# Performance work log

Hardware: AMD Instinct MI355X
Metric: run time of the kernel (lower is better)

Reference implementation:

```python
import jax, jax.numpy as jnp
import numpy as np
from jax import lax

GO_ID = 2
EOS_ID = 3
MAX_LEN = 64
BATCH = 32
VOCAB = 32000
EMBED = 256
HIDDEN = 512


def setup_inputs() -> dict:
    key = jax.random.key(0)
    ks = jax.random.split(key, 8)
    s = 0.05  # keep logits / gates in a sane range
    return {
        "emb_table": jax.random.normal(ks[0], (VOCAB, EMBED), jnp.float32) * s,
        "W_ih": jax.random.normal(ks[1], (3 * HIDDEN, EMBED), jnp.float32) * s,
        "b_ih": jax.random.normal(ks[2], (3 * HIDDEN,), jnp.float32) * s,
        "W_hh": jax.random.normal(ks[3], (3 * HIDDEN, HIDDEN), jnp.float32) * s,
        "b_hh": jax.random.normal(ks[4], (3 * HIDDEN,), jnp.float32) * s,
        "W_out": jax.random.normal(ks[5], (VOCAB, HIDDEN), jnp.float32) * s,
        "b_out": jax.random.normal(ks[6], (VOCAB,), jnp.float32) * s,
        "h0": jax.random.normal(ks[7], (BATCH, HIDDEN), jnp.float32),
    }


def reference(emb_table, W_ih, b_ih, W_hh, b_hh, W_out, b_out, h0):
    start_id = GO_ID  # no_unk=True -> start_id = dm.go_id

    def gru_cell(x, h):
        # torch.nn.GRUCell semantics
        gi = x @ W_ih.T + b_ih            # [B, 3H]
        gh = h @ W_hh.T + b_hh            # [B, 3H]
        i_r, i_z, i_n = jnp.split(gi, 3, axis=-1)
        h_r, h_z, h_n = jnp.split(gh, 3, axis=-1)
        r = jax.nn.sigmoid(i_r + h_r)
        z = jax.nn.sigmoid(i_z + h_z)
        n = jnp.tanh(i_n + r * h_n)
        return (1.0 - z) * n + z * h

    first_emb = jnp.broadcast_to(emb_table[GO_ID], (BATCH, EMBED))
    flag0 = jnp.zeros((BATCH,), dtype=bool)

    def step(carry, _):
        h, next_emb, flag = carry
        h = gru_cell(next_emb, h)
        w = h @ W_out.T + b_out                      # logits [B, V]
        w_pro = jax.nn.softmax(w, axis=-1)
        tok = jnp.argmax(w[:, start_id:], axis=1) + start_id  # greedy, skip specials
        ne = emb_table[tok]
        eosmet = flag                                 # flag BEFORE updating (as in torch loop)
        flag = flag | (tok == EOS_ID)
        return (h, ne, flag), (w_pro, tok, ne, eosmet)

    _, (w_pro, w_o, emb_seq, EOSmet) = lax.scan(
        step, (h0, first_emb, flag0), None, length=MAX_LEN
    )
    alive = jnp.logical_not(EOSmet)                   # EOSmet = 1 - stacked flags
    w_o = w_o * alive.astype(w_o.dtype)               # zero out tokens after EOS
    emb_seq = emb_seq * alive.astype(emb_seq.dtype)[..., None]
    length = jnp.sum(alive.astype(jnp.int32), axis=0)
    return w_pro, w_o, emb_seq, length
```

## Files before the change

### kernel.cpp

```cpp
#include <hip/hip_runtime.h>
#include <math.h>

#define BB 32
#define EE 256
#define HH 512
#define VV 32000
#define TT 64
#define GO_ID 2
#define EOS_ID 3

#define NBL 500
#define NT  256

#define WS_HT0   0
#define WS_HT1   16384
#define WS_X     32768
#define WS_PART  40960
#define WS_M     104960
#define WS_SINV  104992
#define WS_INT   105024

#define OUT_WO   65536000ULL
#define OUT_EMB  (OUT_WO + 2048ULL)
#define OUT_LEN  (OUT_EMB + 524288ULL)

__global__ __launch_bounds__(NT)
void k_init(const float* __restrict__ emb, float* __restrict__ ws)
{
    float* xbuf = ws + WS_X;
    int* toki  = (int*)(ws + WS_INT);
    int* flags = toki;
    int* lenac = toki + 32;
    xbuf[blockIdx.x*EE + threadIdx.x] = emb[GO_ID*EE + threadIdx.x];
    if (blockIdx.x == 0 && threadIdx.x < BB) { flags[threadIdx.x] = 0; lenac[threadIdx.x] = 0; }
}

__global__ __launch_bounds__(NT)
void k_gru(const float* __restrict__ Wih, const float* __restrict__ bih,
           const float* __restrict__ Whh, const float* __restrict__ bhh,
           const float* __restrict__ h0, float* __restrict__ ws, int t)
{
    const int blk = blockIdx.x, tid = threadIdx.x;
    float* hTprev = ws + (((t & 1) == 0) ? WS_HT1 : WS_HT0);
    float* hTcur  = ws + (((t & 1) == 0) ? WS_HT0 : WS_HT1);
    const float* xbuf = ws + WS_X;

    __shared__ float smem[1536];

    const int b    = tid & 31;
    const int q    = tid >> 5;
    const int k    = blk*4 + (q & 3);
    const int half = q >> 2;

    float s_ir = 0.f, s_iz = 0.f, s_in = 0.f;
    {
        const float4* x4 = (const float4*)xbuf + b*64;
        const float4* wr = (const float4*)Wih + (size_t)k*64;
        const float4* wz = (const float4*)Wih + (size_t)(HH + k)*64;
        const float4* wn = (const float4*)Wih + (size_t)(2*HH + k)*64;
        const int c0 = half*32, c1 = c0 + 32;
        for (int c4 = c0; c4 < c1; ++c4) {
            float4 xv = x4[c4];
            float4 a  = wr[c4];
            s_ir += a.x*xv.x + a.y*xv.y + a.z*xv.z + a.w*xv.w;
            float4 bz = wz[c4];
            s_iz += bz.x*xv.x + bz.y*xv.y + bz.z*xv.z + bz.w*xv.w;
            float4 cn = wn[c4];
            s_in += cn.x*xv.x + cn.y*xv.y + cn.z*xv.z + cn.w*xv.w;
        }
    }
    float s_hr = 0.f, s_hz = 0.f, s_hn = 0.f;
    {
        const float4* wr = (const float4*)Whh + (size_t)k*128;
        const float4* wz = (const float4*)Whh + (size_t)(HH + k)*128;
        const float4* wn = (const float4*)Whh + (size_t)(2*HH + k)*128;
        const int c0 = half*64, c1 = c0 + 64;
        if (t == 0) {
            const float4* h4 = (const float4*)h0 + b*128;
            for (int c4 = c0; c4 < c1; ++c4) {
                float4 hv = h4[c4];
                float4 a  = wr[c4];
                s_hr += a.x*hv.x + a.y*hv.y + a.z*hv.z + a.w*hv.w;
                float4 bz = wz[c4];
                s_hz += bz.x*hv.x + bz.y*hv.y + bz.z*hv.z + bz.w*hv.w;
                float4 cn = wn[c4];
                s_hn += cn.x*hv.x + cn.y*hv.y + cn.z*hv.z + cn.w*hv.w;
            }
        } else {
            const float4* h4 = (const float4*)hTprev;
            for (int c4 = c0; c4 < c1; ++c4) {
                float4 hv = h4[c4*32 + b];
                float4 a  = wr[c4];
                s_hr += a.x*hv.x + a.y*hv.y + a.z*hv.z + a.w*hv.w;
                float4 bz = wz[c4];
                s_hz += bz.x*hv.x + bz.y*hv.y + bz.z*hv.z + bz.w*hv.w;
                float4 cn = wn[c4];
                s_hn += cn.x*hv.x + cn.y*hv.y + cn.z*hv.z + cn.w*hv.w;
            }
        }
    }
    const int si = (q*32 + b)*6;
    smem[si+0] = s_ir; smem[si+1] = s_iz; smem[si+2] = s_in;
    smem[si+3] = s_hr; smem[si+4] = s_hz; smem[si+5] = s_hn;
    __syncthreads();
    if (q < 4) {
        const int i0 = (q*32 + b)*6, i1 = ((q+4)*32 + b)*6;
        float ir  = smem[i0+0] + smem[i1+0] + bih[k];
        float iz  = smem[i0+1] + smem[i1+1] + bih[HH + k];
        float inn = smem[i0+2] + smem[i1+2] + bih[2*HH + k];
        float hr  = smem[i0+3] + smem[i1+3] + bhh[k];
        float hz  = smem[i0+4] + smem[i1+4] + bhh[HH + k];
        float hn  = smem[i0+5] + smem[i1+5] + bhh[2*HH + k];
        float r = 1.f/(1.f + expf(-(ir + hr)));
        float z = 1.f/(1.f + expf(-(iz + hz)));
        float n = tanhf(inn + r*hn);
        float hp = (t == 0) ? h0[b*HH + k] : hTprev[(k>>2)*128 + b*4 + (k&3)];
        float hv = (1.f - z)*n + z*hp;
        hTcur[(k>>2)*128 + b*4 + (k&3)] = hv;
    }
}

__global__ __launch_bounds__(NT)
void k_logits(const float* __restrict__ Wout, const float* __restrict__ bout,
              float* __restrict__ out, float* __restrict__ ws, int t)
{
    const int blk = blockIdx.x, tid = threadIdx.x;
    const float* hTcur = ws + (((t & 1) == 0) ? WS_HT0 : WS_HT1);
    float* part  = ws + WS_PART;
    const float* Mrow  = ws + WS_M;
    const float* SinvA = ws + WS_SINV;
    float* w_pro = out;

    __shared__ float smem[2080];

    if (t > 0) {
        float* wp = w_pro + (size_t)(t-1)*1024000 + blk*64;
        const int vl = tid & 63, bq = tid >> 6;
        #pragma unroll
        for (int r = 0; r < 8; ++r) {
            int b = r*4 + bq;
            size_t idx = (size_t)b*VV + vl;
            wp[idx] = expf(wp[idx] - Mrow[b]) * SinvA[b];
        }
    }

    const int b  = tid & 31;
    const int vg = tid >> 5;
    const int v0 = blk*64 + vg*8;
    float acc[8] = {0.f,0.f,0.f,0.f,0.f,0.f,0.f,0.f};
    const float4* hT4  = (const float4*)hTcur;
    const float4* wrow = (const float4*)Wout + (size_t)v0*128;
    for (int c4 = 0; c4 < 128; ++c4) {
        float4 hv = hT4[c4*32 + b];
        #pragma unroll
        for (int i = 0; i < 8; ++i) {
            float4 wv = wrow[(size_t)i*128 + c4];
            acc[i] += wv.x*hv.x + wv.y*hv.y + wv.z*hv.z + wv.w*hv.w;
        }
    }
    __syncthreads();
    #pragma unroll
    for (int i = 0; i < 8; ++i)
        smem[b*65 + vg*8 + i] = acc[i] + bout[v0 + i];
    __syncthreads();
    {
        float* wp = w_pro + (size_t)t*1024000 + blk*64;
        const int vl = tid & 63, bq = tid >> 6;
        #pragma unroll
        for (int r = 0; r < 8; ++r) {
            int b2 = r*4 + bq;
            wp[(size_t)b2*VV + vl] = smem[b2*65 + vl];
        }
    }
    {
        const int rb = tid >> 3, l = tid & 7;
        float m = -INFINITY, s = 0.f, av = -INFINITY; int ai = 0;
        for (int j = l; j < 64; j += 8) {
            float val = smem[rb*65 + j];
            if (val > m) { s = s*expf(m - val) + 1.f; m = val; }
            else         { s += expf(val - m); }
            int vglob = blk*64 + j;
            if (vglob >= 2 && val > av) { av = val; ai = vglob; }
        }
        for (int d = 1; d < 8; d <<= 1) {
            float m2  = __shfl_xor(m, d);
            float s2  = __shfl_xor(s, d);
            float av2 = __shfl_xor(av, d);
            int   ai2 = __shfl_xor(ai, d);
            float mn = fmaxf(m, m2);
            s = s*expf(m - mn) + s2*expf(m2 - mn); m = mn;
            if (av2 > av || (av2 == av && ai2 < ai)) { av = av2; ai = ai2; }
        }
        if (l == 0)
            ((float4*)part)[blk*32 + rb] = make_float4(m, s, av, __int_as_float(ai));
    }
}

__global__ __launch_bounds__(NT)
void k_reduce(const float* __restrict__ emb, float* __restrict__ out,
              float* __restrict__ ws, int t)
{
    const int b = blockIdx.x, tid = threadIdx.x;
    const float* part = ws + WS_PART;
    float* Mrow  = ws + WS_M;
    float* SinvA = ws + WS_SINV;
    int*   flags = (int*)(ws + WS_INT);
    int*   lenac = flags + 32;
    float* xbuf  = ws + WS_X;

    float* w_o    = out + OUT_WO;
    float* emb_sq = out + OUT_EMB;
    float* len_o  = out + OUT_LEN;

    __shared__ float smem[32];

    float m = -INFINITY, s = 0.f, av = -INFINITY; int ai = 0;
    for (int j = tid; j < NBL; j += NT) {
        float4 p = ((const float4*)part)[j*32 + b];
        float mn = fmaxf(m, p.x);
        s = s*expf(m - mn) + p.y*expf(p.x - mn); m = mn;
        int aij = __float_as_int(p.w);
        if (p.z > av || (p.z == av && aij < ai)) { av = p.z; ai = aij; }
    }
    for (int d = 1; d < 64; d <<= 1) {
        float m2  = __shfl_xor(m, d);
        float s2  = __shfl_xor(s, d);
        float av2 = __shfl_xor(av, d);
        int   ai2 = __shfl_xor(ai, d);
        float mn = fmaxf(m, m2);
        s = s*expf(m - mn) + s2*expf(m2 - mn); m = mn;
        if (av2 > av || (av2 == av && ai2 < ai)) { av = av2; ai = ai2; }
    }
    const int wid = tid >> 6, lane = tid & 63;
    if (lane == 0) {
        smem[wid*4+0] = m; smem[wid*4+1] = s;
        smem[wid*4+2] = av; smem[wid*4+3] = __int_as_float(ai);
    }
    __syncthreads();
    if (tid == 0) {
        float M = smem[0], S = smem[1], AV = smem[2];
        int AI = __float_as_int(smem[3]);
        for (int w2 = 1; w2 < 4; ++w2) {
            float m2 = smem[w2*4], s2 = smem[w2*4+1], av2 = smem[w2*4+2];
            int ai2 = __float_as_int(smem[w2*4+3]);
            float mn = fmaxf(M, m2);
            S = S*expf(M - mn) + s2*expf(m2 - mn); M = mn;
            if (av2 > AV || (av2 == AV && ai2 < AI)) { AV = av2; AI = ai2; }
        }
        Mrow[b] = M; SinvA[b] = 1.f/S;
        int fl = flags[b];
        int alive = fl ? 0 : 1;
        w_o[t*BB + b] = alive ? (float)AI : 0.f;
        flags[b] = fl | (AI == EOS_ID ? 1 : 0);
        lenac[b] += alive;
        if (t == TT-1) len_o[b] = (float)lenac[b];
        smem[16] = __int_as_float(AI);
        smem[17] = (float)alive;
    }
    __syncthreads();
    const int tok = __float_as_int(smem[16]);
    const float alive = smem[17];
    float e = emb[(size_t)tok*EE + tid];
    xbuf[b*EE + tid] = e;
    emb_sq[(size_t)t*8192 + b*EE + tid] = alive * e;
}

__global__ __launch_bounds__(NT)
void k_norm_last(float* __restrict__ out, float* __restrict__ ws)
{
    const int blk = blockIdx.x, tid = threadIdx.x;
    const float* Mrow  = ws + WS_M;
    const float* SinvA = ws + WS_SINV;
    float* wp = out + (size_t)(TT-1)*1024000 + blk*64;
    const int vl = tid & 63, bq = tid >> 6;
    #pragma unroll
    for (int r = 0; r < 8; ++r) {
        int b = r*4 + bq;
        size_t idx = (size_t)b*VV + vl;
        wp[idx] = expf(wp[idx] - Mrow[b]) * SinvA[b];
    }
}

extern "C" void kernel_launch(void* const* d_in, const int* in_sizes, int n_in,
                              void* d_out, int out_size, void* d_ws, size_t ws_size,
                              hipStream_t stream)
{
    const float* emb  = (const float*)d_in[0];
    const float* Wih  = (const float*)d_in[1];
    const float* bih  = (const float*)d_in[2];
    const float* Whh  = (const float*)d_in[3];
    const float* bhh  = (const float*)d_in[4];
    const float* Wout = (const float*)d_in[5];
    const float* bout = (const float*)d_in[6];
    const float* h0   = (const float*)d_in[7];
    float* out = (float*)d_out;
    float* ws  = (float*)d_ws;

    hipLaunchKernelGGL(k_init, dim3(BB), dim3(NT), 0, stream, emb, ws);
    for (int t = 0; t < TT; ++t) {
        hipLaunchKernelGGL(k_gru,    dim3(128), dim3(NT), 0, stream, Wih, bih, Whh, bhh, h0, ws, t);
        hipLaunchKernelGGL(k_logits, dim3(NBL), dim3(NT), 0, stream, Wout, bout, out, ws, t);
        hipLaunchKernelGGL(k_reduce, dim3(BB),  dim3(NT), 0, stream, emb, out, ws, t);
    }
    hipLaunchKernelGGL(k_norm_last, dim3(NBL), dim3(NT), 0, stream, out, ws);
}
```

Baseline: 7.078 ms.

## Fuse decoder steps into one persistent cooperative kernel with grid syncs

Replaces the per-step sequence of GRU, logits and reduction launches with a single cooperative kernel that loops over all time steps, using grid-wide syncs between phases. Softmax normalization of the previous step's logits is folded into the next step's pass, and the GRU input is gathered directly from the embedding table by token. This removes launch overhead and intermediate kernels. In exchange it adds two grid barriers per step, needs all blocks co-resident, and runs with large 1024-thread blocks. A fallback path keeps the old multi-kernel launch if the cooperative launch fails.

```diff
diff --git a/kernel.cpp b/kernel.cpp
--- a/kernel.cpp
+++ b/kernel.cpp
@@ -1,5 +1,8 @@
 #include <hip/hip_runtime.h>
+#include <hip/hip_cooperative_groups.h>
 #include <math.h>
+
+namespace cg = cooperative_groups;
 
 #define BB 32
 #define EE 256
@@ -9,9 +12,263 @@
 #define GO_ID 2
 #define EOS_ID 3
 
+#define CNB 250
+#define CNT 1024
+
+#define OUT_WO   65536000ULL
+#define OUT_EMB  (OUT_WO + 2048ULL)
+#define OUT_LEN  (OUT_EMB + 524288ULL)
+
+__device__ __forceinline__ void merge_sm(float& m, float& s, float& av, int& ai,
+                                         float m2, float s2, float av2, int ai2)
+{
+    float mn = fmaxf(m, m2);
+    s = s*expf(m - mn) + s2*expf(m2 - mn);
+    m = mn;
+    if (av2 > av || (av2 == av && ai2 < ai)) { av = av2; ai = ai2; }
+}
+
+struct SmemT {
+    float  logitS[32*129];
+    float4 redS[CNT];
+    float  gruS[CNT*6];
+    float  mprev[32];
+    float  sprev[32];
+    int    toksS[32];
+    int    flagsS;
+};
+
+__device__ __forceinline__ void gru_phase(
+    int bk, int tid, bool init, const int* toks,
+    const float* __restrict__ emb,
+    const float* __restrict__ Wih, const float* __restrict__ bih,
+    const float* __restrict__ Whh, const float* __restrict__ bhh,
+    const float* __restrict__ h0, const float* __restrict__ hprevT,
+    float* __restrict__ hTout, float* __restrict__ gruS)
+{
+    const int b   = tid & 31;
+    const int q   = tid >> 5;
+    const int ko  = q & 3;
+    const int seg = q >> 2;
+    const int k   = bk*4 + ko;
+    const int tok = init ? GO_ID : toks[b];
+
+    float s_ir = 0.f, s_iz = 0.f, s_in = 0.f;
+    {
+        const float4* x4 = (const float4*)emb + (size_t)tok*64;
+        const float4* wr = (const float4*)Wih + (size_t)k*64;
+        const float4* wz = (const float4*)Wih + (size_t)(HH + k)*64;
+        const float4* wn = (const float4*)Wih + (size_t)(2*HH + k)*64;
+        #pragma unroll
+        for (int i = 0; i < 8; ++i) {
+            int c = seg*8 + i;
+            float4 xv = x4[c];
+            float4 a  = wr[c]; s_ir += a.x*xv.x + a.y*xv.y + a.z*xv.z + a.w*xv.w;
+            float4 bz = wz[c]; s_iz += bz.x*xv.x + bz.y*xv.y + bz.z*xv.z + bz.w*xv.w;
+            float4 cn = wn[c]; s_in += cn.x*xv.x + cn.y*xv.y + cn.z*xv.z + cn.w*xv.w;
+        }
+    }
+    float s_hr = 0.f, s_hz = 0.f, s_hn = 0.f;
+    {
+        const float4* wr = (const float4*)Whh + (size_t)k*128;
+        const float4* wz = (const float4*)Whh + (size_t)(HH + k)*128;
+        const float4* wn = (const float4*)Whh + (size_t)(2*HH + k)*128;
+        const float4* h4 = init ? ((const float4*)h0 + b*128) : ((const float4*)hprevT);
+        #pragma unroll
+        for (int i = 0; i < 16; ++i) {
+            int c = seg*16 + i;
+            float4 hv = init ? h4[c] : h4[c*32 + b];
+            float4 a  = wr[c]; s_hr += a.x*hv.x + a.y*hv.y + a.z*hv.z + a.w*hv.w;
+            float4 bz = wz[c]; s_hz += bz.x*hv.x + bz.y*hv.y + bz.z*hv.z + bz.w*hv.w;
+            float4 cn = wn[c]; s_hn += cn.x*hv.x + cn.y*hv.y + cn.z*hv.z + cn.w*hv.w;
+        }
+    }
+    const int si = (q*32 + b)*6;
+    gruS[si+0] = s_ir; gruS[si+1] = s_iz; gruS[si+2] = s_in;
+    gruS[si+3] = s_hr; gruS[si+4] = s_hz; gruS[si+5] = s_hn;
+    __syncthreads();
+    if (q < 4) {
+        const int kk = bk*4 + q;
+        float ir = bih[kk], iz = bih[HH+kk], inn = bih[2*HH+kk];
+        float hr = bhh[kk], hz = bhh[HH+kk], hn  = bhh[2*HH+kk];
+        #pragma unroll
+        for (int s2 = 0; s2 < 8; ++s2) {
+            int base = ((s2*4 + q)*32 + b)*6;
+            ir  += gruS[base+0]; iz += gruS[base+1]; inn += gruS[base+2];
+            hr  += gruS[base+3]; hz += gruS[base+4]; hn  += gruS[base+5];
+        }
+        float r = 1.f/(1.f + expf(-(ir + hr)));
+        float z = 1.f/(1.f + expf(-(iz + hz)));
+        float n = tanhf(inn + r*hn);
+        float hp = init ? h0[b*HH + kk] : hprevT[(kk>>2)*128 + b*4 + (kk&3)];
+        hTout[(kk>>2)*128 + b*4 + (kk&3)] = (1.f - z)*n + z*hp;
+    }
+}
+
+__global__ __launch_bounds__(CNT, 4)
+void fused_decoder(const float* __restrict__ emb,
+                   const float* __restrict__ Wih, const float* __restrict__ bih,
+                   const float* __restrict__ Whh, const float* __restrict__ bhh,
+                   const float* __restrict__ Wout, const float* __restrict__ bout,
+                   const float* __restrict__ h0,
+                   float* __restrict__ out, float* __restrict__ ws)
+{
+    cg::grid_group grid = cg::this_grid();
+    const int blk = blockIdx.x, tid = threadIdx.x;
+
+    float* hb0 = ws;
+    float* hb1 = ws + 16384;
+    float4* part4 = (float4*)(ws + 32768);
+
+    float* w_pro  = out;
+    float* w_o    = out + OUT_WO;
+    float* emb_sq = out + OUT_EMB;
+    float* len_o  = out + OUT_LEN;
+
+    __shared__ SmemT sm;
+
+    int len_b = 0;
+    if (tid == 0) sm.flagsS = 0;
+    __syncthreads();
+
+    if (blk >= 64 && blk < 192)
+        gru_phase(blk-64, tid, true, sm.toksS, emb, Wih, bih, Whh, bhh, h0, nullptr, hb0, sm.gruS);
+    grid.sync();
+
+    for (int t = 0; t < TT; ++t) {
+        const float* hT = (t & 1) ? hb1 : hb0;
+
+        if (t > 0) {
+            const int vl = tid & 127, bq = tid >> 7;
+            float* wp = w_pro + (size_t)(t-1)*1024000 + (size_t)blk*128;
+            #pragma unroll
+            for (int rr = 0; rr < 4; ++rr) {
+                int b2 = rr*8 + bq;
+                size_t idx = (size_t)b2*VV + vl;
+                wp[idx] = expf(wp[idx] - sm.mprev[b2]) * sm.sprev[b2];
+            }
+        }
+        {
+            const int b = tid & 31, vg = tid >> 5;
+            const int v0 = blk*128 + vg*4;
+            float a0=0.f, a1=0.f, a2=0.f, a3=0.f;
+            const float4* hT4 = (const float4*)hT;
+            const float4* w0 = (const float4*)Wout + (size_t)v0*128;
+            const float4* w1 = w0 + 128;
+            const float4* w2 = w0 + 256;
+            const float4* w3 = w0 + 384;
+            for (int c4 = 0; c4 < 128; ++c4) {
+                float4 hv = hT4[c4*32 + b];
+                float4 p;
+                p = w0[c4]; a0 += p.x*hv.x + p.y*hv.y + p.z*hv.z + p.w*hv.w;
+                p = w1[c4]; a1 += p.x*hv.x + p.y*hv.y + p.z*hv.z + p.w*hv.w;
+                p = w2[c4]; a2 += p.x*hv.x + p.y*hv.y + p.z*hv.z + p.w*hv.w;
+                p = w3[c4]; a3 += p.x*hv.x + p.y*hv.y + p.z*hv.z + p.w*hv.w;
+            }
+            sm.logitS[b*129 + vg*4 + 0] = a0 + bout[v0+0];
+            sm.logitS[b*129 + vg*4 + 1] = a1 + bout[v0+1];
+            sm.logitS[b*129 + vg*4 + 2] = a2 + bout[v0+2];
+            sm.logitS[b*129 + vg*4 + 3] = a3 + bout[v0+3];
+        }
+        __syncthreads();
+        {
+            const int vl = tid & 127, bq = tid >> 7;
+            float* wp = w_pro + (size_t)t*1024000 + (size_t)blk*128;
+            #pragma unroll
+            for (int rr = 0; rr < 4; ++rr) {
+                int b2 = rr*8 + bq;
+                wp[(size_t)b2*VV + vl] = sm.logitS[b2*129 + vl];
+            }
+        }
+        {
+            const int b = tid & 31, l = tid >> 5;
+            float m=-INFINITY, s=0.f, av=-INFINITY; int ai=0;
+            #pragma unroll
+            for (int i = 0; i < 4; ++i) {
+                int j = l + (i<<5);
+                float val = sm.logitS[b*129 + j];
+                if (val > m) { s = s*expf(m - val) + 1.f; m = val; }
+                else         { s += expf(val - m); }
+                int vglob = blk*128 + j;
+                if (vglob >= 2 && val > av) { av = val; ai = vglob; }
+            }
+            sm.redS[tid] = make_float4(m, s, av, __int_as_float(ai));
+        }
+        __syncthreads();
+        if (tid < 32) {
+            float4 p0 = sm.redS[tid];
+            float m=p0.x, s=p0.y, av=p0.z; int ai=__float_as_int(p0.w);
+            for (int jj = 1; jj < 32; ++jj) {
+                float4 p = sm.redS[tid + (jj<<5)];
+                merge_sm(m, s, av, ai, p.x, p.y, p.z, __float_as_int(p.w));
+            }
+            part4[blk*32 + tid] = make_float4(m, s, av, __int_as_float(ai));
+        }
+        grid.sync();
+
+        {
+            const int b = tid & 31, jg = tid >> 5;
+            float m=-INFINITY, s=0.f, av=-INFINITY; int ai=0;
+            #pragma unroll
+            for (int i = 0; i < 8; ++i) {
+                int j = jg + (i<<5);
+                if (j < CNB) {
+                    float4 p = part4[j*32 + b];
+                    merge_sm(m, s, av, ai, p.x, p.y, p.z, __float_as_int(p.w));
+                }
+            }
+            sm.redS[tid] = make_float4(m, s, av, __int_as_float(ai));
+        }
+        __syncthreads();
+        if (tid < 32) {
+            float4 p0 = sm.redS[tid];
+            float m=p0.x, s=p0.y, av=p0.z; int ai=__float_as_int(p0.w);
+            for (int jj = 1; jj < 32; ++jj) {
+                float4 p = sm.redS[tid + (jj<<5)];
+                merge_sm(m, s, av, ai, p.x, p.y, p.z, __float_as_int(p.w));
+            }
+            sm.mprev[tid] = m;
+            sm.sprev[tid] = 1.f/s;
+            sm.toksS[tid] = ai;
+        }
+        __syncthreads();
+        const int oldflags = sm.flagsS;
+        __syncthreads();
+        {
+            unsigned long long bal = __ballot((tid < 32) && (sm.toksS[tid & 31] == EOS_ID));
+            if (tid == 0) sm.flagsS = oldflags | (int)(bal & 0xFFFFFFFFull);
+        }
+        if (blk < 32) {
+            const int tok   = sm.toksS[blk];
+            const int alive = ((oldflags >> blk) & 1) ^ 1;
+            if (tid == 0) w_o[t*BB + blk] = alive ? (float)tok : 0.f;
+            len_b += alive;
+            if (tid < EE) {
+                float e = alive ? emb[(size_t)tok*EE + tid] : 0.f;
+                emb_sq[(size_t)t*8192 + blk*EE + tid] = e;
+            }
+            if (t == TT-1 && tid == 32) len_o[blk] = (float)len_b;
+        }
+        if (t < TT-1 && blk >= 64 && blk < 192)
+            gru_phase(blk-64, tid, false, sm.toksS, emb, Wih, bih, Whh, bhh, h0,
+                      (t & 1) ? hb1 : hb0, (t & 1) ? hb0 : hb1, sm.gruS);
+        grid.sync();
+    }
+
+    {
+        const int vl = tid & 127, bq = tid >> 7;
+        float* wp = w_pro + (size_t)(TT-1)*1024000 + (size_t)blk*128;
+        #pragma unroll
+        for (int rr = 0; rr < 4; ++rr) {
+            int b2 = rr*8 + bq;
+            size_t idx = (size_t)b2*VV + vl;
+            wp[idx] = expf(wp[idx] - sm.mprev[b2]) * sm.sprev[b2];
+        }
+    }
+}
+
 #define NBL 500
 #define NT  256
-
 #define WS_HT0   0
 #define WS_HT1   16384
 #define WS_X     32768
@@ -20,10 +277,6 @@
 #define WS_SINV  104992
 #define WS_INT   105024
 
-#define OUT_WO   65536000ULL
-#define OUT_EMB  (OUT_WO + 2048ULL)
-#define OUT_LEN  (OUT_EMB + 524288ULL)
-
 __global__ __launch_bounds__(NT)
 void k_init(const float* __restrict__ emb, float* __restrict__ ws)
 {
@@ -61,12 +314,9 @@
         const int c0 = half*32, c1 = c0 + 32;
         for (int c4 = c0; c4 < c1; ++c4) {
             float4 xv = x4[c4];
-            float4 a  = wr[c4];
-            s_ir += a.x*xv.x + a.y*xv.y + a.z*xv.z + a.w*xv.w;
-            float4 bz = wz[c4];
-            s_iz += bz.x*xv.x + bz.y*xv.y + bz.z*xv.z + bz.w*xv.w;
-            float4 cn = wn[c4];
-            s_in += cn.x*xv.x + cn.y*xv.y + cn.z*xv.z + cn.w*xv.w;
+            float4 a  = wr[c4]; s_ir += a.x*xv.x + a.y*xv.y + a.z*xv.z + a.w*xv.w;
+            float4 bz = wz[c4]; s_iz += bz.x*xv.x + bz.y*xv.y + bz.z*xv.z + bz.w*xv.w;
+            float4 cn = wn[c4]; s_in += cn.x*xv.x + cn.y*xv.y + cn.z*xv.z + cn.w*xv.w;
         }
     }
     float s_hr = 0.f, s_hz = 0.f, s_hn = 0.f;
@@ -79,23 +329,17 @@
             const float4* h4 = (const float4*)h0 + b*128;
             for (int c4 = c0; c4 < c1; ++c4) {
                 float4 hv = h4[c4];
-                float4 a  = wr[c4];
-                s_hr += a.x*hv.x + a.y*hv.y + a.z*hv.z + a.w*hv.w;
-                float4 bz = wz[c4];
-                s_hz += bz.x*hv.x + bz.y*hv.y + bz.z*hv.z + bz.w*hv.w;
-                float4 cn = wn[c4];
-                s_hn += cn.x*hv.x + cn.y*hv.y + cn.z*hv.z + cn.w*hv.w;
+                float4 a  = wr[c4]; s_hr += a.x*hv.x + a.y*hv.y + a.z*hv.z + a.w*hv.w;
+                float4 bz = wz[c4]; s_hz += bz.x*hv.x + bz.y*hv.y + bz.z*hv.z + bz.w*hv.w;
+                float4 cn = wn[c4]; s_hn += cn.x*hv.x + cn.y*hv.y + cn.z*hv.z + cn.w*hv.w;
             }
         } else {
             const float4* h4 = (const float4*)hTprev;
             for (int c4 = c0; c4 < c1; ++c4) {
                 float4 hv = h4[c4*32 + b];
-                float4 a  = wr[c4];
-                s_hr += a.x*hv.x + a.y*hv.y + a.z*hv.z + a.w*hv.w;
-                float4 bz = wz[c4];
-                s_hz += bz.x*hv.x + bz.y*hv.y + bz.z*hv.z + bz.w*hv.w;
-                float4 cn = wn[c4];
-                s_hn += cn.x*hv.x + cn.y*hv.y + cn.z*hv.z + cn.w*hv.w;
+                float4 a  = wr[c4]; s_hr += a.x*hv.x + a.y*hv.y + a.z*hv.z + a.w*hv.w;
+                float4 bz = wz[c4]; s_hz += bz.x*hv.x + bz.y*hv.y + bz.z*hv.z + bz.w*hv.w;
+                float4 cn = wn[c4]; s_hn += cn.x*hv.x + cn.y*hv.y + cn.z*hv.z + cn.w*hv.w;
             }
         }
     }
@@ -296,11 +540,18 @@
     float* out = (float*)d_out;
     float* ws  = (float*)d_ws;
 
-    hipLaunchKernelGGL(k_init, dim3(BB), dim3(NT), 0, stream, emb, ws);
-    for (int t = 0; t < TT; ++t) {
-        hipLaunchKernelGGL(k_gru,    dim3(128), dim3(NT), 0, stream, Wih, bih, Whh, bhh, h0, ws, t);
-        hipLaunchKernelGGL(k_logits, dim3(NBL), dim3(NT), 0, stream, Wout, bout, out, ws, t);
-        hipLaunchKernelGGL(k_reduce, dim3(BB),  dim3(NT), 0, stream, emb, out, ws, t);
-    }
-    hipLaunchKernelGGL(k_norm_last, dim3(NBL), dim3(NT), 0, stream, out, ws);
-}
+    void* args[] = { (void*)&emb, (void*)&Wih, (void*)&bih, (void*)&Whh, (void*)&bhh,
+                     (void*)&Wout, (void*)&bout, (void*)&h0, (void*)&out, (void*)&ws };
+    hipError_t err = hipLaunchCooperativeKernel((const void*)fused_decoder,
+                                                dim3(CNB), dim3(CNT), args, 0, stream);
+    if (err != hipSuccess) {
+        (void)hipGetLastError();
+        hipLaunchKernelGGL(k_init, dim3(BB), dim3(NT), 0, stream, emb, ws);
+        for (int t = 0; t < TT; ++t) {
+            hipLaunchKernelGGL(k_gru,    dim3(128), dim3(NT), 0, stream, Wih, bih, Whh, bhh, h0, ws, t);
+            hipLaunchKernelGGL(k_logits, dim3(NBL), dim3(NT), 0, stream, Wout, bout, out, ws, t);
+            hipLaunchKernelGGL(k_reduce, dim3(BB),  dim3(NT), 0, stream, emb, out, ws, t);
+        }
+        hipLaunchKernelGGL(k_norm_last, dim3(NBL), dim3(NT), 0, stream, out, ws);
+    }
+}
```

Measured after the change: 10.36 ms. +46.4%, slower.
